# Kernel optimization log

Measured on AMD Instinct MI355X. Metric: run time of the kernel, lower is better.

Reference implementation:

```python
import jax, jax.numpy as jnp
import numpy as np

N = 8192
BACKBONE_DIM = 384
PCD_FEAT_DIM = 6
OUT_DIM = 384
WIDTH = 384
N_HID_INST = 6
N_HID_POS = 4
MARGIN = 1.0
MAX_GROUPING_SCALE = 2.0
EPS_NORM = 1e-5
EPS_D2 = 1e-12


def setup_inputs() -> dict:
    key = jax.random.key(0)
    ks = jax.random.split(key, 12)
    s = 0.05  # ~1/sqrt(384) fan-in init
    inp = {
        "point_selected_feat": jax.random.normal(ks[0], (N, BACKBONE_DIM), jnp.float32),
        "point_orgfeat": jax.random.normal(ks[1], (N, PCD_FEAT_DIM), jnp.float32),
        "scale": jax.random.uniform(ks[2], (N, 1), jnp.float32, 0.0, 2.0),
        "mask_id": jax.random.randint(ks[3], (N,), 0, 64, jnp.int64 if jax.config.jax_enable_x64 else jnp.int32),
        "rand_u": jax.random.uniform(ks[4], (1,), jnp.float32),
        "chunk_size": 256,
        "inst_W_in": jax.random.normal(ks[5], (BACKBONE_DIM + 1, WIDTH), jnp.float32) * s,
        "inst_W_hid": jax.random.normal(ks[6], (N_HID_INST - 1, WIDTH, WIDTH), jnp.float32) * s,
        "inst_W_out": jax.random.normal(ks[7], (WIDTH, OUT_DIM), jnp.float32) * s,
        "pos_W_in": jax.random.normal(ks[8], (PCD_FEAT_DIM + 1, WIDTH), jnp.float32) * s,
        "pos_W_hid": jax.random.normal(ks[9], (N_HID_POS - 1, WIDTH, WIDTH), jnp.float32) * s,
        "pos_W_out": jax.random.normal(ks[10], (WIDTH, OUT_DIM), jnp.float32) * s,
    }
    return inp


def _mlp(x, W_in, W_hid, W_out):
    h = jax.nn.relu(x @ W_in)
    def body(h, W):
        return jax.nn.relu(h @ W), None
    h, _ = jax.lax.scan(body, h, W_hid)
    return h @ W_out


def _normed(x):
    n = jnp.linalg.norm(x, axis=-1, keepdims=True)
    return x / (n + EPS_NORM)


def _embed(feat_sel, feat_org, s, iWi, iWh, iWo, pWi, pWh, pWo):
    # quantile_transformer is fit externally at runtime; identity here
    inst = _normed(_mlp(jnp.concatenate([feat_sel, s], axis=-1), iWi, iWh, iWo))
    pos = _normed(_mlp(jnp.concatenate([feat_org, s], axis=-1), pWi, pWh, pWo))
    return inst + pos


def _chunk_pdist(emb, C, S):
    # pairwise L2 distances within each chunk via gram trick: [C,S,S]
    z = emb.reshape(C, S, -1)
    sq = jnp.sum(z * z, axis=-1)                      # [C,S]
    g = jnp.einsum("csd,ctd->cst", z, z)              # [C,S,S]
    d2 = sq[:, :, None] + sq[:, None, :] - 2.0 * g
    return jnp.sqrt(jnp.where(d2 > EPS_D2, d2, EPS_D2))


def _masked_mean(vals, mask):
    cnt = jnp.maximum(jnp.sum(mask), 1).astype(vals.dtype)
    return jnp.sum(vals * mask) / cnt


def reference(point_selected_feat, point_orgfeat, scale, mask_id, rand_u, chunk_size,
              inst_W_in, inst_W_hid, inst_W_out, pos_W_in, pos_W_hid, pos_W_out):
    S = chunk_size
    C = point_selected_feat.shape[0] // S

    lab = mask_id.reshape(C, S)
    eq = lab[:, :, None] == lab[:, None, :]                       # label equality within chunk
    valid = lab != -1
    valid_pair = valid[:, :, None] & valid[:, None, :]
    triu = jnp.triu(jnp.ones((S, S), dtype=bool), k=0)            # block_mask after triu(diag=0)
    block = triu[None] & valid_pair                               # [C,S,S]
    diag = jnp.eye(S, dtype=bool)[None]
    pos_mask = (eq & block & ~diag).astype(jnp.float32)
    neg_mask = ((~eq) & block).astype(jnp.float32)
    sum_block = jnp.sum(block).astype(jnp.float32)

    w_pos = jnp.sum(pos_mask) / sum_block
    w_neg = jnp.sum(neg_mask) / sum_block

    args = (inst_W_in, inst_W_hid, inst_W_out, pos_W_in, pos_W_hid, pos_W_out)

    # loss 1 (and loss 3 reuses the same embedding: original recomputes identically)
    emb = _embed(point_selected_feat, point_orgfeat, scale, *args)
    dist = _chunk_pdist(emb, C, S)
    loss1 = _masked_mean(dist, pos_mask)
    loss3 = _masked_mean(jax.nn.relu(MARGIN - dist), neg_mask)

    # hierarchy loss at a randomly enlarged scale
    scale_diff = jnp.maximum(0.0, MAX_GROUPING_SCALE - scale)
    larger_scale = scale + scale_diff * rand_u
    emb2 = _embed(point_selected_feat, point_orgfeat, larger_scale, *args)
    dist2 = _chunk_pdist(emb2, C, S)
    loss2 = _masked_mean(dist2, pos_mask)

    total = loss1 * w_pos + loss2 * w_pos + loss3 * w_neg
    return total
```

## Files before the change

### kernel.cpp

```cpp
#include <hip/hip_runtime.h>
#include <math.h>

#define NPTS 8192
#define DIMW 384
#define MB   64
#define LDH  424
#define KIN  416
#define KPOS 32
#define SCH  256
#define NCH  32
#define LZB  136
#define EWAVES 12
#define ETHREADS (EWAVES * 64)

typedef __attribute__((ext_vector_type(8))) short bf16x8;
typedef __attribute__((ext_vector_type(4))) float f32x4;
typedef __attribute__((ext_vector_type(4))) unsigned short us4;
typedef __attribute__((ext_vector_type(8))) unsigned short us8;

#define SZ_HID   (384*384)
#define OFF_IIN  0
#define SZ_IIN   (384*416)
#define OFF_IHID (OFF_IIN + SZ_IIN)
#define OFF_IOUT (OFF_IHID + 5*SZ_HID)
#define OFF_PIN  (OFF_IOUT + SZ_HID)
#define SZ_PIN   (384*32)
#define OFF_PHID (OFF_PIN + SZ_PIN)
#define OFF_POUT (OFF_PHID + 3*SZ_HID)
#define WTS_USHORTS (OFF_POUT + SZ_HID)
#define WTS_BYTES   ((size_t)WTS_USHORTS * 2)
#define EMB_US      ((size_t)NPTS * DIMW)
#define EMB_BYTES   (EMB_US * 2)

__device__ __forceinline__ ushort f2bf(float x) {
  union { float f; unsigned u; } v; v.f = x;
  unsigned r = v.u + 0x7FFF + ((v.u >> 16) & 1);
  return (ushort)(r >> 16);
}
__device__ __forceinline__ float bf2f(ushort u) {
  union { unsigned u; float f; } v; v.u = ((unsigned)u) << 16; return v.f;
}

__global__ __launch_bounds__(256) void convert_wts_swz(
    const float* __restrict__ iWin, const float* __restrict__ iWhid,
    const float* __restrict__ iWout, const float* __restrict__ pWin,
    const float* __restrict__ pWhid, const float* __restrict__ pWout,
    ushort* __restrict__ wts) {
  const int seg = blockIdx.y;
  const float* src; ushort* dst; int Ksrc, NKl;
  if (seg == 0)      { src = iWin;  dst = wts + OFF_IIN;  Ksrc = 385; NKl = 13; }
  else if (seg <= 5) { src = iWhid + (size_t)(seg-1)*SZ_HID; dst = wts + OFF_IHID + (size_t)(seg-1)*SZ_HID; Ksrc = 384; NKl = 12; }
  else if (seg == 6) { src = iWout; dst = wts + OFF_IOUT; Ksrc = 384; NKl = 12; }
  else if (seg == 7) { src = pWin;  dst = wts + OFF_PIN;  Ksrc = 7;   NKl = 1;  }
  else if (seg <= 10){ src = pWhid + (size_t)(seg-8)*SZ_HID; dst = wts + OFF_PHID + (size_t)(seg-8)*SZ_HID; Ksrc = 384; NKl = 12; }
  else               { src = pWout; dst = wts + OFF_POUT; Ksrc = 384; NKl = 12; }
  const int t = blockIdx.x * 256 + threadIdx.x;
  if (t >= NKl * 1536) return;
  const int lane = t & 63;
  const int frag = t >> 6;
  const int i = frag & 1;
  const int rest = frag >> 1;
  const int ks = rest % NKl;
  const int wave = rest / NKl;
  const int n  = wave * 32 + i * 16 + (lane & 15);
  const int kb = ks * 32 + (lane >> 4) * 8;
  us8 o;
#pragma unroll
  for (int e = 0; e < 8; ++e) {
    const int k = kb + e;
    o[e] = (k < Ksrc) ? f2bf(src[(size_t)k * 384 + n]) : (ushort)0;
  }
  *(us8*)&dst[(size_t)t * 8] = o;
}

template <int KW, bool STORE>
__device__ __forceinline__ void mlayer(const ushort* __restrict__ Wt,
    const ushort* __restrict__ bin, ushort* __restrict__ bout,
    int wave, int lane, int lr, int lq, int n0, f32x4 acc[2][4]) {
  constexpr int NK = KW / 32;
#pragma unroll
  for (int i = 0; i < 2; ++i)
#pragma unroll
    for (int j = 0; j < 4; ++j) acc[i][j] = (f32x4)(0.f);

  bf16x8 w[5][2], h[2][4];
  const ushort* wp = Wt + (size_t)wave * NK * 1024 + lane * 8;
  const ushort* hp = bin + lr * LDH + lq * 8;

#pragma unroll
  for (int d = 0; d < 4; ++d) {
    if (d < NK) {
#pragma unroll
      for (int i = 0; i < 2; ++i)
        w[d][i] = *(const bf16x8*)(wp + d * 1024 + i * 512);
    }
  }
#pragma unroll
  for (int j = 0; j < 4; ++j) h[0][j] = *(const bf16x8*)(hp + j * 16 * LDH);

#pragma unroll
  for (int ks = 0; ks < NK; ++ks) {
    if (ks + 4 < NK) {
#pragma unroll
      for (int i = 0; i < 2; ++i)
        w[(ks + 4) % 5][i] = *(const bf16x8*)(wp + (ks + 4) * 1024 + i * 512);
    }
    if (ks + 1 < NK) {
#pragma unroll
      for (int j = 0; j < 4; ++j)
        h[(ks + 1) & 1][j] = *(const bf16x8*)(hp + j * 16 * LDH + (ks + 1) * 32);
    }
#pragma unroll
    for (int j = 0; j < 4; ++j)
#pragma unroll
      for (int i = 0; i < 2; ++i)
        acc[i][j] = __builtin_amdgcn_mfma_f32_16x16x32_bf16(w[ks % 5][i], h[ks & 1][j], acc[i][j], 0, 0, 0);
  }
  if (STORE) {
#pragma unroll
    for (int i = 0; i < 2; ++i)
#pragma unroll
      for (int j = 0; j < 4; ++j) {
        f32x4 a = acc[i][j];
        us4 o;
        o[0] = f2bf(fmaxf(a[0], 0.f));
        o[1] = f2bf(fmaxf(a[1], 0.f));
        o[2] = f2bf(fmaxf(a[2], 0.f));
        o[3] = f2bf(fmaxf(a[3], 0.f));
        *(us4*)&bout[(j * 16 + lr) * LDH + n0 + i * 16 + lq * 4] = o;
      }
    __syncthreads();
  }
}

__device__ __forceinline__ void norm_store(f32x4 acc[2][4], ushort* __restrict__ embp,
    bool add, int lr, int lq, int wave, int n0, float (*wsum)[64], float* invn) {
#pragma unroll
  for (int j = 0; j < 4; ++j) {
    float s = 0.f;
#pragma unroll
    for (int i = 0; i < 2; ++i) {
      f32x4 a = acc[i][j];
      s = fmaf(a[0], a[0], s); s = fmaf(a[1], a[1], s);
      s = fmaf(a[2], a[2], s); s = fmaf(a[3], a[3], s);
    }
    s += __shfl_xor(s, 16, 64);
    s += __shfl_xor(s, 32, 64);
    if (lq == 0) wsum[wave][j * 16 + lr] = s;
  }
  __syncthreads();
  if (threadIdx.x < 64) {
    float tot = 0.f;
#pragma unroll
    for (int w = 0; w < EWAVES; ++w) tot += wsum[w][threadIdx.x];
    invn[threadIdx.x] = 1.f / (sqrtf(tot) + 1e-5f);
  }
  __syncthreads();
#pragma unroll
  for (int j = 0; j < 4; ++j) {
    const float inv = invn[j * 16 + lr];
#pragma unroll
    for (int i = 0; i < 2; ++i) {
      ushort* p = embp + (size_t)(j * 16 + lr) * DIMW + n0 + i * 16 + lq * 4;
      float o0 = acc[i][j][0] * inv, o1 = acc[i][j][1] * inv;
      float o2 = acc[i][j][2] * inv, o3 = acc[i][j][3] * inv;
      if (add) {
        us4 old = *(const us4*)p;
        o0 += bf2f(old[0]); o1 += bf2f(old[1]);
        o2 += bf2f(old[2]); o3 += bf2f(old[3]);
      }
      us4 o; o[0] = f2bf(o0); o[1] = f2bf(o1); o[2] = f2bf(o2); o[3] = f2bf(o3);
      *(us4*)p = o;
    }
  }
  __syncthreads();
}

__global__ __launch_bounds__(ETHREADS) void embed_mfma(
    const float* __restrict__ feat_sel, const float* __restrict__ feat_org,
    const float* __restrict__ scale, const float* __restrict__ rand_u,
    const ushort* __restrict__ wts, ushort* __restrict__ emb) {
  __shared__ ushort bufA[MB * LDH];
  __shared__ ushort bufB[MB * LDH];
  __shared__ float s_lds[MB];
  __shared__ float wsum[EWAVES][64];
  __shared__ float invn[64];

  const int t = threadIdx.x;
  const int p0 = blockIdx.x * MB;
  const int var = blockIdx.y;
  ushort* embp = emb + (size_t)var * EMB_US + (size_t)p0 * DIMW;

  if (t < MB) {
    float s = scale[p0 + t];
    if (var) s += fmaxf(0.f, 2.f - s) * rand_u[0];
    s_lds[t] = s;
  }
#pragma unroll
  for (int it = 0; it < 8; ++it) {
    int idx = t + it * ETHREADS;
    int m = idx / 96, kq = idx - m * 96;
    const float4 v = *(const float4*)&feat_sel[(size_t)(p0 + m) * DIMW + kq * 4];
    us4 o; o[0] = f2bf(v.x); o[1] = f2bf(v.y); o[2] = f2bf(v.z); o[3] = f2bf(v.w);
    *(us4*)&bufA[m * LDH + kq * 4] = o;
  }
  if (t < MB) {
    bufA[t * LDH + 384] = f2bf(s_lds[t]);
#pragma unroll
    for (int k = 385; k < KIN; ++k) bufA[t * LDH + k] = 0;
  }
  __syncthreads();

  const int lane = t & 63, wave = t >> 6;
  const int lr = lane & 15, lq = lane >> 4;
  const int n0 = wave * 32;
  f32x4 acc[2][4];

  mlayer<KIN,  true >(wts + OFF_IIN,             bufA, bufB, wave, lane, lr, lq, n0, acc);
  mlayer<DIMW, true >(wts + OFF_IHID + 0*SZ_HID, bufB, bufA, wave, lane, lr, lq, n0, acc);
  mlayer<DIMW, true >(wts + OFF_IHID + 1*SZ_HID, bufA, bufB, wave, lane, lr, lq, n0, acc);
  mlayer<DIMW, true >(wts + OFF_IHID + 2*SZ_HID, bufB, bufA, wave, lane, lr, lq, n0, acc);
  mlayer<DIMW, true >(wts + OFF_IHID + 3*SZ_HID, bufA, bufB, wave, lane, lr, lq, n0, acc);
  mlayer<DIMW, true >(wts + OFF_IHID + 4*SZ_HID, bufB, bufA, wave, lane, lr, lq, n0, acc);
  mlayer<DIMW, false>(wts + OFF_IOUT,            bufA, bufB, wave, lane, lr, lq, n0, acc);
  norm_store(acc, embp, false, lr, lq, wave, n0, wsum, invn);

  if (t < MB) {
    const float* fo = feat_org + (size_t)(p0 + t) * 6;
    ushort* r = bufA + t * LDH;
#pragma unroll
    for (int k = 0; k < 6; ++k) r[k] = f2bf(fo[k]);
    r[6] = f2bf(s_lds[t]);
#pragma unroll
    for (int k = 7; k < KPOS; ++k) r[k] = 0;
  }
  __syncthreads();

  mlayer<KPOS, true >(wts + OFF_PIN,             bufA, bufB, wave, lane, lr, lq, n0, acc);
  mlayer<DIMW, true >(wts + OFF_PHID + 0*SZ_HID, bufB, bufA, wave, lane, lr, lq, n0, acc);
  mlayer<DIMW, true >(wts + OFF_PHID + 1*SZ_HID, bufA, bufB, wave, lane, lr, lq, n0, acc);
  mlayer<DIMW, true >(wts + OFF_PHID + 2*SZ_HID, bufB, bufA, wave, lane, lr, lq, n0, acc);
  mlayer<DIMW, false>(wts + OFF_POUT,            bufA, bufB, wave, lane, lr, lq, n0, acc);
  norm_store(acc, embp, true, lr, lq, wave, n0, wsum, invn);
}

__global__ __launch_bounds__(512) void dist_mfma(
    const ushort* __restrict__ emb, const int* __restrict__ mask_id,
    float* __restrict__ part) {
  __shared__ ushort zb[SCH * LZB];
  __shared__ float sqv[SCH];
  __shared__ int labv[SCH];
  __shared__ float scratch[8];

  const int c = blockIdx.x, hh = blockIdx.y, v = blockIdx.z;
  const int t = threadIdx.x;
  const ushort* embc = emb + (size_t)v * EMB_US + (size_t)c * SCH * DIMW;

  if (t < SCH) labv[t] = mask_id[c * SCH + t];

  const int lane = t & 63, wave = t >> 6;
  const int lr = lane & 15, lq = lane >> 4;
  const int wa = wave >> 2, wb = wave & 3;

  f32x4 acc[4][4];
#pragma unroll
  for (int i = 0; i < 4; ++i)
#pragma unroll
    for (int j = 0; j < 4; ++j) acc[i][j] = (f32x4)(0.f);

  const int sr = t >> 1, sh = (t & 1) * 64;
  float sq = 0.f;

  for (int kc = 0; kc < 3; ++kc) {
    __syncthreads();
    const ushort* zrow = embc + (size_t)sr * DIMW + kc * 128 + sh;
    ushort* zd = zb + sr * LZB + sh;
#pragma unroll
    for (int q = 0; q < 8; ++q) {
      us8 x = *(const us8*)&zrow[q * 8];
      *(us8*)&zd[q * 8] = x;
#pragma unroll
      for (int e = 0; e < 8; ++e) { float f = bf2f(x[e]); sq = fmaf(f, f, sq); }
    }
    __syncthreads();
    const ushort* ap = zb + (hh * 128 + wa * 64 + lr) * LZB + lq * 8;
    const ushort* bp = zb + (wb * 64 + lr) * LZB + lq * 8;
#pragma unroll
    for (int ks = 0; ks < 4; ++ks) {
      bf16x8 af[4], bfr[4];
#pragma unroll
      for (int i = 0; i < 4; ++i) af[i] = *(const bf16x8*)(ap + i * 16 * LZB + ks * 32);
#pragma unroll
      for (int j = 0; j < 4; ++j) bfr[j] = *(const bf16x8*)(bp + j * 16 * LZB + ks * 32);
#pragma unroll
      for (int j = 0; j < 4; ++j)
#pragma unroll
        for (int i = 0; i < 4; ++i)
          acc[i][j] = __builtin_amdgcn_mfma_f32_16x16x32_bf16(af[i], bfr[j], acc[i][j], 0, 0, 0);
    }
  }
  sq += __shfl_xor(sq, 1, 64);
  if (!(t & 1)) sqv[sr] = sq;
  __syncthreads();

  float s_pos = 0.f, s_neg = 0.f, c_pos = 0.f, c_neg = 0.f, c_blk = 0.f;
#pragma unroll
  for (int i = 0; i < 4; ++i) {
    const int ib = hh * 128 + wa * 64 + i * 16 + lq * 4;
#pragma unroll
    for (int j = 0; j < 4; ++j) {
      const int jG = wb * 64 + j * 16 + lr;
      const int lj = labv[jG];
      const float sqj = sqv[jG];
#pragma unroll
      for (int vv = 0; vv < 4; ++vv) {
        const int iG = ib + vv;
        const int li = labv[iG];
        if (li != -1 && lj != -1 && iG <= jG) {
          c_blk += 1.f;
          if (iG < jG) {
            float d2 = sqv[iG] + sqj - 2.f * acc[i][j][vv];
            float d = sqrtf(fmaxf(d2, 1e-12f));
            if (li == lj) { s_pos += d; c_pos += 1.f; }
            else          { s_neg += fmaxf(1.f - d, 0.f); c_neg += 1.f; }
          }
        }
      }
    }
  }
  float vals[5] = { s_pos, s_neg, c_pos, c_neg, c_blk };
  float res[5];
#pragma unroll
  for (int r = 0; r < 5; ++r) {
    float x = vals[r];
#pragma unroll
    for (int o = 32; o > 0; o >>= 1) x += __shfl_xor(x, o, 64);
    __syncthreads();
    if ((t & 63) == 0) scratch[t >> 6] = x;
    __syncthreads();
    float s = 0.f;
#pragma unroll
    for (int w = 0; w < 8; ++w) s += scratch[w];
    res[r] = s;
  }
  if (t == 0) {
    float* pb = part + (size_t)((v * 2 + hh) * NCH + c) * 8;
    pb[0] = res[0]; pb[1] = res[1]; pb[2] = res[2]; pb[3] = res[3]; pb[4] = res[4];
  }
}

__global__ __launch_bounds__(128) void final_kernel(
    const float* __restrict__ part, float* __restrict__ out) {
  __shared__ float scratch[2];
  const int t = threadIdx.x;
  const float* pb = part + (size_t)t * 8;
  const bool v0 = t < 64;
  float sp1 = v0 ? pb[0] : 0.f;
  float sp2 = v0 ? 0.f : pb[0];
  float sn  = v0 ? pb[1] : 0.f;
  float cp  = v0 ? pb[2] : 0.f;
  float cn  = v0 ? pb[3] : 0.f;
  float cb  = v0 ? pb[4] : 0.f;
  float vals[6] = { sp1, sp2, sn, cp, cn, cb };
  float res[6];
#pragma unroll
  for (int r = 0; r < 6; ++r) {
    float x = vals[r];
#pragma unroll
    for (int o = 32; o > 0; o >>= 1) x += __shfl_xor(x, o, 64);
    __syncthreads();
    if ((t & 63) == 0) scratch[t >> 6] = x;
    __syncthreads();
    res[r] = scratch[0] + scratch[1];
  }
  if (t == 0) {
    float l1 = res[0] / fmaxf(res[3], 1.f);
    float l2 = res[1] / fmaxf(res[3], 1.f);
    float l3 = res[2] / fmaxf(res[4], 1.f);
    out[0] = (l1 + l2) * (res[3] / res[5]) + l3 * (res[4] / res[5]);
  }
}

extern "C" void kernel_launch(void* const* d_in, const int* in_sizes, int n_in,
                              void* d_out, int out_size, void* d_ws, size_t ws_size,
                              hipStream_t stream) {
  const float* feat_sel = (const float*)d_in[0];
  const float* feat_org = (const float*)d_in[1];
  const float* scale    = (const float*)d_in[2];
  const int*   mask_id  = (const int*)d_in[3];
  const float* rand_u   = (const float*)d_in[4];
  const float* iWin  = (const float*)d_in[6];
  const float* iWhid = (const float*)d_in[7];
  const float* iWout = (const float*)d_in[8];
  const float* pWin  = (const float*)d_in[9];
  const float* pWhid = (const float*)d_in[10];
  const float* pWout = (const float*)d_in[11];

  ushort* wts = (ushort*)d_ws;
  ushort* emb = (ushort*)((char*)d_ws + WTS_BYTES);
  float*  part = (float*)((char*)d_ws + WTS_BYTES + 2 * EMB_BYTES);

  dim3 gC(78, 12);
  convert_wts_swz<<<gC, 256, 0, stream>>>(iWin, iWhid, iWout, pWin, pWhid, pWout, wts);

  dim3 gE(NPTS / MB, 2);
  embed_mfma<<<gE, ETHREADS, 0, stream>>>(feat_sel, feat_org, scale, rand_u, wts, emb);

  dim3 gD(NCH, 2, 2);
  dist_mfma<<<gD, 512, 0, stream>>>(emb, mask_id, part);

  final_kernel<<<1, 128, 0, stream>>>(part, (float*)d_out);
}
```

Baseline: 105.5 us.

## Swizzle MLP activation LDS layout and batch weight prefetch in groups of four

Activation tiles in shared memory are now stored with an XOR swizzle on 16-byte slots, keyed by row, to cut LDS bank conflicts on MFMA operand reads. The row pitch grows to 448. The weight prefetch changes from a 5-deep rolling ring to double-buffered chunks of four k-steps. Launch bounds now request 3 blocks per CU. The larger LDS footprint and the extra registers for the double-buffered weights may limit occupancy or cause spills.

```diff
diff --git a/kernel.cpp b/kernel.cpp
--- a/kernel.cpp
+++ b/kernel.cpp
@@ -4,7 +4,7 @@
 #define NPTS 8192
 #define DIMW 384
 #define MB   64
-#define LDH  424
+#define LDH  448
 #define KIN  416
 #define KPOS 32
 #define SCH  256
@@ -73,48 +73,57 @@
   *(us8*)&dst[(size_t)t * 8] = o;
 }
 
-template <int KW, bool STORE>
+template <int NK, bool STORE>
 __device__ __forceinline__ void mlayer(const ushort* __restrict__ Wt,
     const ushort* __restrict__ bin, ushort* __restrict__ bout,
     int wave, int lane, int lr, int lq, int n0, f32x4 acc[2][4]) {
-  constexpr int NK = KW / 32;
 #pragma unroll
   for (int i = 0; i < 2; ++i)
 #pragma unroll
     for (int j = 0; j < 4; ++j) acc[i][j] = (f32x4)(0.f);
 
-  bf16x8 w[5][2], h[2][4];
+  constexpr int NC = (NK + 3) / 4;
+  bf16x8 w[2][4][2], h[2][4];
   const ushort* wp = Wt + (size_t)wave * NK * 1024 + lane * 8;
-  const ushort* hp = bin + lr * LDH + lq * 8;
-
-#pragma unroll
-  for (int d = 0; d < 4; ++d) {
-    if (d < NK) {
+  const int swz = lr & 7;
+  const ushort* hbase = bin + lr * LDH;
+
+#pragma unroll
+  for (int s = 0; s < 4; ++s)
+    if (s < NK)
 #pragma unroll
       for (int i = 0; i < 2; ++i)
-        w[d][i] = *(const bf16x8*)(wp + d * 1024 + i * 512);
-    }
-  }
-#pragma unroll
-  for (int j = 0; j < 4; ++j) h[0][j] = *(const bf16x8*)(hp + j * 16 * LDH);
-
-#pragma unroll
-  for (int ks = 0; ks < NK; ++ks) {
-    if (ks + 4 < NK) {
-#pragma unroll
-      for (int i = 0; i < 2; ++i)
-        w[(ks + 4) % 5][i] = *(const bf16x8*)(wp + (ks + 4) * 1024 + i * 512);
-    }
-    if (ks + 1 < NK) {
-#pragma unroll
-      for (int j = 0; j < 4; ++j)
-        h[(ks + 1) & 1][j] = *(const bf16x8*)(hp + j * 16 * LDH + (ks + 1) * 32);
-    }
-#pragma unroll
-    for (int j = 0; j < 4; ++j)
-#pragma unroll
-      for (int i = 0; i < 2; ++i)
-        acc[i][j] = __builtin_amdgcn_mfma_f32_16x16x32_bf16(w[ks % 5][i], h[ks & 1][j], acc[i][j], 0, 0, 0);
+        w[0][s][i] = *(const bf16x8*)(wp + s * 1024 + i * 512);
+#pragma unroll
+  for (int j = 0; j < 4; ++j)
+    h[0][j] = *(const bf16x8*)(hbase + j * 16 * LDH + ((lq ^ swz) << 3));
+
+#pragma unroll
+  for (int c = 0; c < NC; ++c) {
+    if (c + 1 < NC) {
+#pragma unroll
+      for (int s = 0; s < 4; ++s)
+        if ((c + 1) * 4 + s < NK)
+#pragma unroll
+          for (int i = 0; i < 2; ++i)
+            w[(c + 1) & 1][s][i] = *(const bf16x8*)(wp + (size_t)((c + 1) * 4 + s) * 1024 + i * 512);
+    }
+#pragma unroll
+    for (int s = 0; s < 4; ++s) {
+      const int ks = c * 4 + s;
+      if (ks < NK) {
+        if (ks + 1 < NK) {
+#pragma unroll
+          for (int j = 0; j < 4; ++j)
+            h[(ks + 1) & 1][j] = *(const bf16x8*)(hbase + j * 16 * LDH + ((((ks + 1) * 4 + lq) ^ swz) << 3));
+        }
+#pragma unroll
+        for (int j = 0; j < 4; ++j)
+#pragma unroll
+          for (int i = 0; i < 2; ++i)
+            acc[i][j] = __builtin_amdgcn_mfma_f32_16x16x32_bf16(w[c & 1][s][i], h[ks & 1][j], acc[i][j], 0, 0, 0);
+      }
+    }
   }
   if (STORE) {
 #pragma unroll
@@ -127,7 +136,9 @@
         o[1] = f2bf(fmaxf(a[1], 0.f));
         o[2] = f2bf(fmaxf(a[2], 0.f));
         o[3] = f2bf(fmaxf(a[3], 0.f));
-        *(us4*)&bout[(j * 16 + lr) * LDH + n0 + i * 16 + lq * 4] = o;
+        const int col = n0 + i * 16 + lq * 4;
+        const int slot = col >> 3;
+        *(us4*)&bout[(j * 16 + lr) * LDH + (((slot ^ swz) << 3) | ((lq & 1) << 2))] = o;
       }
     __syncthreads();
   }
@@ -176,7 +187,7 @@
   __syncthreads();
 }
 
-__global__ __launch_bounds__(ETHREADS) void embed_mfma(
+__global__ __launch_bounds__(ETHREADS, 3) void embed_mfma(
     const float* __restrict__ feat_sel, const float* __restrict__ feat_org,
     const float* __restrict__ scale, const float* __restrict__ rand_u,
     const ushort* __restrict__ wts, ushort* __restrict__ emb) {
@@ -202,12 +213,14 @@
     int m = idx / 96, kq = idx - m * 96;
     const float4 v = *(const float4*)&feat_sel[(size_t)(p0 + m) * DIMW + kq * 4];
     us4 o; o[0] = f2bf(v.x); o[1] = f2bf(v.y); o[2] = f2bf(v.z); o[3] = f2bf(v.w);
-    *(us4*)&bufA[m * LDH + kq * 4] = o;
+    const int ph = (((kq >> 1) ^ (m & 7)) << 3) | ((kq & 1) << 2);
+    *(us4*)&bufA[m * LDH + ph] = o;
   }
   if (t < MB) {
-    bufA[t * LDH + 384] = f2bf(s_lds[t]);
-#pragma unroll
-    for (int k = 385; k < KIN; ++k) bufA[t * LDH + k] = 0;
+    us8 z = (us8)(0);
+#pragma unroll
+    for (int q = 48; q < 56; ++q) *(us8*)&bufA[t * LDH + q * 8] = z;
+    bufA[t * LDH + 384 + (t & 7) * 8] = f2bf(s_lds[t]);
   }
   __syncthreads();
 
@@ -216,31 +229,36 @@
   const int n0 = wave * 32;
   f32x4 acc[2][4];
 
-  mlayer<KIN,  true >(wts + OFF_IIN,             bufA, bufB, wave, lane, lr, lq, n0, acc);
-  mlayer<DIMW, true >(wts + OFF_IHID + 0*SZ_HID, bufB, bufA, wave, lane, lr, lq, n0, acc);
-  mlayer<DIMW, true >(wts + OFF_IHID + 1*SZ_HID, bufA, bufB, wave, lane, lr, lq, n0, acc);
-  mlayer<DIMW, true >(wts + OFF_IHID + 2*SZ_HID, bufB, bufA, wave, lane, lr, lq, n0, acc);
-  mlayer<DIMW, true >(wts + OFF_IHID + 3*SZ_HID, bufA, bufB, wave, lane, lr, lq, n0, acc);
-  mlayer<DIMW, true >(wts + OFF_IHID + 4*SZ_HID, bufB, bufA, wave, lane, lr, lq, n0, acc);
-  mlayer<DIMW, false>(wts + OFF_IOUT,            bufA, bufB, wave, lane, lr, lq, n0, acc);
+  mlayer<13, true >(wts + OFF_IIN,             bufA, bufB, wave, lane, lr, lq, n0, acc);
+  mlayer<12, true >(wts + OFF_IHID + 0*SZ_HID, bufB, bufA, wave, lane, lr, lq, n0, acc);
+  mlayer<12, true >(wts + OFF_IHID + 1*SZ_HID, bufA, bufB, wave, lane, lr, lq, n0, acc);
+  mlayer<12, true >(wts + OFF_IHID + 2*SZ_HID, bufB, bufA, wave, lane, lr, lq, n0, acc);
+  mlayer<12, true >(wts + OFF_IHID + 3*SZ_HID, bufA, bufB, wave, lane, lr, lq, n0, acc);
+  mlayer<12, true >(wts + OFF_IHID + 4*SZ_HID, bufB, bufA, wave, lane, lr, lq, n0, acc);
+  mlayer<12, false>(wts + OFF_IOUT,            bufA, bufB, wave, lane, lr, lq, n0, acc);
   norm_store(acc, embp, false, lr, lq, wave, n0, wsum, invn);
 
   if (t < MB) {
     const float* fo = feat_org + (size_t)(p0 + t) * 6;
-    ushort* r = bufA + t * LDH;
-#pragma unroll
-    for (int k = 0; k < 6; ++k) r[k] = f2bf(fo[k]);
-    r[6] = f2bf(s_lds[t]);
-#pragma unroll
-    for (int k = 7; k < KPOS; ++k) r[k] = 0;
-  }
-  __syncthreads();
-
-  mlayer<KPOS, true >(wts + OFF_PIN,             bufA, bufB, wave, lane, lr, lq, n0, acc);
-  mlayer<DIMW, true >(wts + OFF_PHID + 0*SZ_HID, bufB, bufA, wave, lane, lr, lq, n0, acc);
-  mlayer<DIMW, true >(wts + OFF_PHID + 1*SZ_HID, bufA, bufB, wave, lane, lr, lq, n0, acc);
-  mlayer<DIMW, true >(wts + OFF_PHID + 2*SZ_HID, bufB, bufA, wave, lane, lr, lq, n0, acc);
-  mlayer<DIMW, false>(wts + OFF_POUT,            bufA, bufB, wave, lane, lr, lq, n0, acc);
+    us8 b0;
+#pragma unroll
+    for (int k = 0; k < 6; ++k) b0[k] = f2bf(fo[k]);
+    b0[6] = f2bf(s_lds[t]);
+    b0[7] = 0;
+    us8 z = (us8)(0);
+    const int e = t & 7;
+    *(us8*)&bufA[t * LDH + ((0 ^ e) << 3)] = b0;
+    *(us8*)&bufA[t * LDH + ((1 ^ e) << 3)] = z;
+    *(us8*)&bufA[t * LDH + ((2 ^ e) << 3)] = z;
+    *(us8*)&bufA[t * LDH + ((3 ^ e) << 3)] = z;
+  }
+  __syncthreads();
+
+  mlayer<1,  true >(wts + OFF_PIN,             bufA, bufB, wave, lane, lr, lq, n0, acc);
+  mlayer<12, true >(wts + OFF_PHID + 0*SZ_HID, bufB, bufA, wave, lane, lr, lq, n0, acc);
+  mlayer<12, true >(wts + OFF_PHID + 1*SZ_HID, bufA, bufB, wave, lane, lr, lq, n0, acc);
+  mlayer<12, true >(wts + OFF_PHID + 2*SZ_HID, bufB, bufA, wave, lane, lr, lq, n0, acc);
+  mlayer<12, false>(wts + OFF_POUT,            bufA, bufB, wave, lane, lr, lq, n0, acc);
   norm_store(acc, embp, true, lr, lq, wave, n0, wsum, invn);
 }
 
```

After: 106.1 us. No clear change (+0.6%).
